# Performance work log

Measured on AMD Instinct MI355X. Metric: run time of the kernel, lower is better.

Reference implementation:

```python
import jax, jax.numpy as jnp
import numpy as np

N, D, K = 8192, 4096, 8
F_HID = D // 4  # 1024


def setup_inputs() -> dict:
    key = jax.random.key(0)
    ks = jax.random.split(key, 8)
    s1 = 1.0 / np.sqrt(2 * D)
    s2 = 1.0 / np.sqrt(F_HID)
    sr = 1.0 / np.sqrt(D)
    return {
        "h_anchor": jax.random.normal(ks[0], (N, D), jnp.float32),
        "h_mask": jax.random.normal(ks[1], (N, D), jnp.float32),
        "Wr": jax.random.normal(ks[2], (K, D), jnp.float32) * sr,
        "br": jnp.zeros((K,), jnp.float32),
        "W1": jax.random.normal(ks[3], (K, F_HID, 2 * D), jnp.float32) * s1,
        "b1": jnp.zeros((K, F_HID), jnp.float32),
        "W2": jax.random.normal(ks[4], (K, D, F_HID), jnp.float32) * s2,
        "b2": jnp.zeros((K, D), jnp.float32),
    }


def reference(h_anchor, h_mask, Wr, br, W1, b1, W2, b2):
    # routing weights: softmax(h_mask @ Wr^T + br) -> [N, K]
    weights = jax.nn.softmax(h_mask @ Wr.T + br, axis=-1)
    # conditioned input: [N, 2D]
    conditioned = jnp.concatenate([h_anchor, h_mask], axis=-1)
    # all-expert first GEMM: [K, N, F]
    h1 = jnp.einsum("nc,kfc->knf", conditioned, W1) + b1[:, None, :]
    h1 = jax.nn.gelu(h1, approximate=False)  # torch nn.GELU default = exact erf
    # second GEMM: [K, N, D]
    expert_out = jnp.einsum("knf,kdf->knd", h1, W2) + b2[:, None, :]
    # softmax-weighted combine over experts -> [N, D]
    return jnp.einsum("knd,nk->nd", expert_out, weights)
```

## Files before the change

### kernel.cpp

```cpp
#include <hip/hip_runtime.h>
#include <hip/hip_bf16.h>
#include <math.h>

typedef __bf16 bf16_t;
typedef __bf16 bf16x4 __attribute__((ext_vector_type(4)));
typedef __bf16 bf16x8 __attribute__((ext_vector_type(8)));
typedef float  f32x4  __attribute__((ext_vector_type(4)));
typedef float  f32x16 __attribute__((ext_vector_type(16)));

#define AS1 __attribute__((address_space(1)))
#define AS3 __attribute__((address_space(3)))

__device__ __forceinline__ void gload_lds16(const bf16_t* g, char* l) {
  __builtin_amdgcn_global_load_lds((const AS1 void*)g, (AS3 void*)l, 16, 0, 0);
}

static constexpr int N_ROWS = 8192;
static constexpr int DDIM   = 4096;
static constexpr int KEXP   = 8;
static constexpr int FHID   = 1024;
static constexpr int KD     = 8192;
static constexpr int NKT    = KD / 64;


__global__ __launch_bounds__(256)
void routing_kernel(const float* __restrict__ hm, const float* __restrict__ Wr,
                    const float* __restrict__ br, float* __restrict__ wgt) {
  const int n = blockIdx.x;
  const int t = threadIdx.x;
  const int wid = t >> 6;
  const float4* row = (const float4*)(hm + (size_t)n * DDIM);
  float4 x[4];
#pragma unroll
  for (int j = 0; j < 4; ++j) x[j] = row[t + j * 256];
  __shared__ float red[KEXP][4];
  float part[KEXP];
#pragma unroll
  for (int k = 0; k < KEXP; ++k) {
    const float4* wr = (const float4*)(Wr + (size_t)k * DDIM);
    float s = 0.f;
#pragma unroll
    for (int j = 0; j < 4; ++j) {
      float4 w4 = wr[t + j * 256];
      s += x[j].x * w4.x + x[j].y * w4.y + x[j].z * w4.z + x[j].w * w4.w;
    }
#pragma unroll
    for (int off = 32; off > 0; off >>= 1) s += __shfl_down(s, off);
    part[k] = s;
  }
  if ((t & 63) == 0) {
#pragma unroll
    for (int k = 0; k < KEXP; ++k) red[k][wid] = part[k];
  }
  __syncthreads();
  if (t == 0) {
    float lg[KEXP];
    float mx = -1e30f;
#pragma unroll
    for (int k = 0; k < KEXP; ++k) {
      lg[k] = red[k][0] + red[k][1] + red[k][2] + red[k][3] + br[k];
      mx = fmaxf(mx, lg[k]);
    }
    float sum = 0.f;
#pragma unroll
    for (int k = 0; k < KEXP; ++k) { lg[k] = expf(lg[k] - mx); sum += lg[k]; }
    float inv = 1.f / sum;
#pragma unroll
    for (int k = 0; k < KEXP; ++k) wgt[(size_t)n * KEXP + k] = lg[k] * inv;
  }
}

__device__ __forceinline__ bf16x4 cvt4(float4 v) {
  bf16x4 o;
  o[0] = (bf16_t)v.x; o[1] = (bf16_t)v.y; o[2] = (bf16_t)v.z; o[3] = (bf16_t)v.w;
  return o;
}

__global__ __launch_bounds__(256)
void pack_cond_kernel(const float* __restrict__ ha, const float* __restrict__ hm,
                      bf16_t* __restrict__ Apk) {
  const int bm = blockIdx.x >> 7, t = blockIdx.x & 127;
  const int tid = threadIdx.x;
  const float* src = (t < 64) ? ha : hm;
  const int cb = (t & 63) * 64;
  __shared__ char pb[32768];
#pragma unroll
  for (int i = 0; i < 16; ++i) {
    int u = i * 256 + tid;
    int r = u >> 4, c = (u & 15) * 4;
    float4 v = *(const float4*)(src + (size_t)(bm * 256 + r) * DDIM + cb + c);
    int off = ((r >> 7) & 1) * 16384 + ((c >> 4) & 3) * 4096 + ((r >> 5) & 3) * 1024
            + ((c >> 3) & 1) * 512 + (r & 31) * 16 + (c & 7) * 2;
    *(bf16x4*)(pb + off) = cvt4(v);
  }
  __syncthreads();
  char* dst = (char*)Apk + (size_t)blockIdx.x * 32768;
#pragma unroll
  for (int i = 0; i < 8; ++i) {
    int off = i * 4096 + tid * 16;
    *(float4*)(dst + off) = *(const float4*)(pb + off);
  }
}

__global__ __launch_bounds__(256)
void pack_w1_kernel(const float* __restrict__ W1, bf16_t* __restrict__ Bpk) {
  const int bn = blockIdx.x >> 7, t = blockIdx.x & 127;
  const int tid = threadIdx.x;
  __shared__ char pb[32768];
#pragma unroll
  for (int i = 0; i < 16; ++i) {
    int u = i * 256 + tid;
    int r = u >> 4, c = (u & 15) * 4;
    float4 v = *(const float4*)(W1 + (size_t)(bn * 256 + r) * KD + t * 64 + c);
    int off = ((c >> 4) & 3) * 8192 + ((r >> 5) & 7) * 1024
            + ((c >> 3) & 1) * 512 + (r & 31) * 16 + (c & 7) * 2;
    *(bf16x4*)(pb + off) = cvt4(v);
  }
  __syncthreads();
  char* dst = (char*)Bpk + (size_t)blockIdx.x * 32768;
#pragma unroll
  for (int i = 0; i < 8; ++i) {
    int off = i * 4096 + tid * 16;
    *(float4*)(dst + off) = *(const float4*)(pb + off);
  }
}

__global__ __launch_bounds__(256)
void pack_w2_kernel(const float* __restrict__ W2, bf16_t* __restrict__ Bpk) {
  const int bn = blockIdx.x >> 7, t = blockIdx.x & 127;
  const int tid = threadIdx.x;
  const int ke = t >> 4, f0 = (t & 15) * 64;
  __shared__ char pb[32768];
#pragma unroll
  for (int i = 0; i < 16; ++i) {
    int u = i * 256 + tid;
    int r = u >> 4, c = (u & 15) * 4;
    float4 v = *(const float4*)(W2 + ((size_t)ke * DDIM + bn * 256 + r) * FHID + f0 + c);
    int off = ((c >> 4) & 3) * 8192 + ((r >> 5) & 7) * 1024
            + ((c >> 3) & 1) * 512 + (r & 31) * 16 + (c & 7) * 2;
    *(bf16x4*)(pb + off) = cvt4(v);
  }
  __syncthreads();
  char* dst = (char*)Bpk + (size_t)blockIdx.x * 32768;
#pragma unroll
  for (int i = 0; i < 8; ++i) {
    int off = i * 4096 + tid * 16;
    *(float4*)(dst + off) = *(const float4*)(pb + off);
  }
}

template <int MODE, int NCOLS>
__global__ __launch_bounds__(512, 2)
void gemm256_kernel(const bf16_t* __restrict__ Apk, const bf16_t* __restrict__ Bpk,
                    void* __restrict__ Cout, const float* __restrict__ bias,
                    const float* __restrict__ wgt) {
  __shared__ char lds_raw[2 * 65536];

  const int tid  = threadIdx.x;
  const int wid  = tid >> 6;
  const int lane = tid & 63;
  const int wr   = wid >> 2;
  const int wc   = wid & 3;

  constexpr int NBN    = NCOLS / 256;
  constexpr int NWIN_N = NBN / 16;
  const int bid = blockIdx.x;
  const int w   = bid >> 8;
  const int sl  = bid & 255;
  const int xcd = sl & 7;
  const int cu  = sl >> 3;
  const int wm  = w / NWIN_N, wn = w % NWIN_N;
  const int bm  = wm * 16 + ((xcd >> 1) << 2) + (cu & 3);
  const int bn  = wn * 16 + ((xcd & 1) << 3) + (cu >> 2);
  const int arow0 = bm * 256;
  const int brow0 = bn * 256;

  const size_t abase = (size_t)bm * NKT * 16384;
  const size_t bbase = (size_t)bn * NKT * 16384;
  const size_t selo  = (size_t)(wid * 512 + lane * 8);
  const int    dsto  = wid << 10;

  f32x16 acc[4][2];
#pragma unroll
  for (int mi = 0; mi < 4; ++mi)
#pragma unroll
    for (int nj = 0; nj < 2; ++nj)
#pragma unroll
      for (int r = 0; r < 16; ++r) acc[mi][nj][r] = 0.f;

#define STG_A(I, TAU, NB)                                                        \
  gload_lds16(Apk + abase + (size_t)((TAU) & (NKT - 1)) * 16384 + (I) * 4096 + selo, \
              (NB) + (I) * 8192 + dsto);
#define STG_B(I, TAU, NB)                                                        \
  gload_lds16(Bpk + bbase + (size_t)((TAU) & (NKT - 1)) * 16384 + (I) * 4096 + selo, \
              (NB) + 32768 + (I) * 8192 + dsto);

  STG_A(0, 0, lds_raw) STG_A(2, 0, lds_raw) STG_B(0, 0, lds_raw) STG_B(1, 0, lds_raw)
  STG_A(1, 0, lds_raw) STG_A(3, 0, lds_raw) STG_B(2, 0, lds_raw) STG_B(3, 0, lds_raw)
  asm volatile("s_waitcnt vmcnt(0)" ::: "memory");
  __builtin_amdgcn_s_barrier();
  __builtin_amdgcn_sched_barrier(0);

#define SB __builtin_amdgcn_sched_barrier(0);
#define MM(MI)                                                                  \
    acc[MI][0] = __builtin_amdgcn_mfma_f32_32x32x16_bf16(aq[MI], qb0,           \
                                                         acc[MI][0], 0, 0, 0);  \
    acc[MI][1] = __builtin_amdgcn_mfma_f32_32x32x16_bf16(aq[MI], qb1,           \
                                                         acc[MI][1], 0, 0, 0);

#define PH(SS, STG0, STG1, GATE)                                                \
  {                                                                             \
    STG0;                                                                       \
    STG1;                                                                       \
    SB                                                                          \
    bf16x8 qb0 = *(const bf16x8*)(bB + (SS) * 8192);                            \
    bf16x8 qb1 = *(const bf16x8*)(bB + (SS) * 8192 + 1024);                     \
    SB                                                                          \
    bf16x8 aq[4];                                                               \
    aq[0] = *(const bf16x8*)(bA + (SS) * 4096);                                 \
    SB                                                                          \
    aq[1] = *(const bf16x8*)(bA + (SS) * 4096 + 1024);                          \
    SB                                                                          \
    aq[2] = *(const bf16x8*)(bA + (SS) * 4096 + 2048);                          \
    SB                                                                          \
    aq[3] = *(const bf16x8*)(bA + (SS) * 4096 + 3072);                          \
    SB                                                                          \
    __builtin_amdgcn_s_setprio(1);                                              \
    asm volatile("s_waitcnt lgkmcnt(3)" ::: "memory");                          \
    SB                                                                          \
    MM(0)                                                                       \
    SB                                                                          \
    asm volatile("s_waitcnt lgkmcnt(2)" ::: "memory");                          \
    SB                                                                          \
    MM(1)                                                                       \
    SB                                                                          \
    asm volatile("s_waitcnt lgkmcnt(1)" ::: "memory");                          \
    SB                                                                          \
    MM(2)                                                                       \
    SB                                                                          \
    asm volatile("s_waitcnt lgkmcnt(0)" ::: "memory");                          \
    SB                                                                          \
    MM(3)                                                                       \
    SB                                                                          \
    __builtin_amdgcn_s_setprio(0);                                              \
    if (GATE) {                                                                 \
      asm volatile("s_waitcnt vmcnt(4)" ::: "memory");                          \
      SB                                                                        \
      __builtin_amdgcn_s_barrier();                                             \
      SB                                                                        \
    }                                                                           \
  }

  int cur = 0;
  for (int t = 0; t < NKT; ++t) {
    char* nb = lds_raw + (cur ^ 65536);
    const char* bA = lds_raw + cur + wr * 16384 + lane * 16;
    const char* bB = lds_raw + cur + 32768 + wc * 2048 + lane * 16;
    PH(0, STG_A(0, t + 1, nb), STG_A(2, t + 1, nb), 0)
    PH(1, STG_B(0, t + 1, nb), STG_B(1, t + 1, nb), 1)
    PH(2, STG_A(1, t + 1, nb), STG_A(3, t + 1, nb), 0)
    PH(3, STG_B(2, t + 1, nb), STG_B(3, t + 1, nb), 1)
    cur ^= 65536;
  }
#undef PH
#undef MM
#undef SB
#undef STG_A
#undef STG_B

  const int rbase = arow0 + wr * 128 + ((lane >> 5) << 2);
  const int cbase = brow0 + wc * 64 + (lane & 31);

  if constexpr (MODE == 1) {
    char* __restrict__ Hc = (char*)Cout;
    const int kexp = brow0 >> 10;
    float bv[2] = {bias[cbase], bias[cbase + 32]};
    size_t cpart[2];
#pragma unroll
    for (int nj = 0; nj < 2; ++nj) {
      int c = cbase + nj * 32;
      cpart[nj] = (size_t)(c >> 6) * 32768 + ((c >> 4) & 3) * 4096
                + ((c >> 3) & 1) * 512 + (c & 7) * 2;
    }
#pragma unroll
    for (int mi = 0; mi < 4; ++mi)
#pragma unroll
      for (int r = 0; r < 16; ++r) {
        int n = rbase + mi * 32 + (r & 3) + 8 * (r >> 2);
        float wn4 = wgt[(size_t)n * KEXP + kexp];
        size_t npart = (size_t)(n >> 8) * (NKT * 32768) + ((n >> 7) & 1) * 16384
                     + ((n >> 5) & 3) * 1024 + (n & 31) * 16;
#pragma unroll
        for (int nj = 0; nj < 2; ++nj) {
          float x = acc[mi][nj][r] + bv[nj];
          float g = 0.5f * x * (1.f + erff(x * 0.70710678118654752f));
          *(bf16_t*)(Hc + npart + cpart[nj]) = (bf16_t)(g * wn4);
        }
      }
  } else {
    float* __restrict__ O = (float*)Cout;
    float bc0[KEXP], bc1[KEXP];
#pragma unroll
    for (int k = 0; k < KEXP; ++k) {
      bc0[k] = bias[(size_t)k * NCOLS + cbase];
      bc1[k] = bias[(size_t)k * NCOLS + cbase + 32];
    }
#pragma unroll
    for (int mi = 0; mi < 4; ++mi)
#pragma unroll
      for (int r = 0; r < 16; ++r) {
        int n = rbase + mi * 32 + (r & 3) + 8 * (r >> 2);
        const float4* wp = (const float4*)(wgt + (size_t)n * KEXP);
        float4 wa = wp[0], wb = wp[1];
        float w8[KEXP] = {wa.x, wa.y, wa.z, wa.w, wb.x, wb.y, wb.z, wb.w};
        float s0 = 0.f, s1 = 0.f;
#pragma unroll
        for (int k = 0; k < KEXP; ++k) { s0 += w8[k] * bc0[k]; s1 += w8[k] * bc1[k]; }
        O[(size_t)n * NCOLS + cbase]      = acc[mi][0][r] + s0;
        O[(size_t)n * NCOLS + cbase + 32] = acc[mi][1][r] + s1;
      }
  }
}

extern "C" void kernel_launch(void* const* d_in, const int* in_sizes, int n_in,
                              void* d_out, int out_size, void* d_ws, size_t ws_size,
                              hipStream_t stream) {
  const float* h_anchor = (const float*)d_in[0];
  const float* h_mask   = (const float*)d_in[1];
  const float* Wr       = (const float*)d_in[2];
  const float* br       = (const float*)d_in[3];
  const float* W1       = (const float*)d_in[4];
  const float* b1       = (const float*)d_in[5];
  const float* W2       = (const float*)d_in[6];
  const float* b2       = (const float*)d_in[7];
  float* out = (float*)d_out;

  char* ws = (char*)d_ws;
  bf16_t* Apk  = (bf16_t*)(ws);
  bf16_t* B1pk = (bf16_t*)(ws + ((size_t)128 << 20));
  bf16_t* B2pk = (bf16_t*)(ws + ((size_t)256 << 20));
  bf16_t* Hpk  = (bf16_t*)(ws + ((size_t)320 << 20));
  float*  wgt  = (float*) (ws + ((size_t)448 << 20));

  routing_kernel<<<N_ROWS, 256, 0, stream>>>(h_mask, Wr, br, wgt);
  pack_cond_kernel<<<32 * 128, 256, 0, stream>>>(h_anchor, h_mask, Apk);
  pack_w1_kernel<<<32 * 128, 256, 0, stream>>>(W1, B1pk);
  pack_w2_kernel<<<16 * 128, 256, 0, stream>>>(W2, B2pk);

  gemm256_kernel<1, 8192><<<(N_ROWS / 256) * (KD / 256), 512, 0, stream>>>(
      Apk, B1pk, (void*)Hpk, b1, wgt);
  gemm256_kernel<2, 4096><<<(N_ROWS / 256) * (DDIM / 256), 512, 0, stream>>>(
      Hpk, B2pk, (void*)out, b2, wgt);
}
```

Measured before the change: 1.639 ms.

## Use 4-wave blocks with 128x128 warp tiles and register double-buffered LDS reads

Halves the GEMM block to 256 threads (4 waves in a 2x2 grid), so each wave computes a 128x128 sub-tile with a 4x4 MFMA accumulator array instead of 4x2. LDS fragments are ping-ponged through two register sets (x/y), and the global-to-LDS staging for the next K tile is interleaved between MFMA groups, with one barrier per K tile. The aim is higher MFMA-to-LDS-read ratio and fewer barriers. In exchange it roughly doubles accumulator register pressure, leaves only 4 waves per CU for latency hiding, and drops the setprio hints.

```diff
diff --git a/kernel.cpp b/kernel.cpp
--- a/kernel.cpp
+++ b/kernel.cpp
@@ -150,7 +150,7 @@
 }
 
 template <int MODE, int NCOLS>
-__global__ __launch_bounds__(512, 2)
+__global__ __launch_bounds__(256, 1)
 void gemm256_kernel(const bf16_t* __restrict__ Apk, const bf16_t* __restrict__ Bpk,
                     void* __restrict__ Cout, const float* __restrict__ bias,
                     const float* __restrict__ wgt) {
@@ -159,8 +159,8 @@
   const int tid  = threadIdx.x;
   const int wid  = tid >> 6;
   const int lane = tid & 63;
-  const int wr   = wid >> 2;
-  const int wc   = wid & 3;
+  const int wr   = wid >> 1;
+  const int wc   = wid & 1;
 
   constexpr int NBN    = NCOLS / 256;
   constexpr int NWIN_N = NBN / 16;
@@ -177,108 +177,119 @@
 
   const size_t abase = (size_t)bm * NKT * 16384;
   const size_t bbase = (size_t)bn * NKT * 16384;
-  const size_t selo  = (size_t)(wid * 512 + lane * 8);
+  const size_t ssub  = (size_t)(wid * 512 + lane * 8);
   const int    dsto  = wid << 10;
 
-  f32x16 acc[4][2];
+  const char* A0 = lds_raw + wr * 16384 + lane * 16;
+  const char* B0 = lds_raw + 32768 + wc * 4096 + lane * 16;
+  const char* A1 = A0 + 65536;
+  const char* B1 = B0 + 65536;
+
+  f32x16 acc[4][4];
 #pragma unroll
   for (int mi = 0; mi < 4; ++mi)
 #pragma unroll
-    for (int nj = 0; nj < 2; ++nj)
+    for (int nj = 0; nj < 4; ++nj)
 #pragma unroll
       for (int r = 0; r < 16; ++r) acc[mi][nj][r] = 0.f;
 
-#define STG_A(I, TAU, NB)                                                        \
-  gload_lds16(Apk + abase + (size_t)((TAU) & (NKT - 1)) * 16384 + (I) * 4096 + selo, \
-              (NB) + (I) * 8192 + dsto);
-#define STG_B(I, TAU, NB)                                                        \
-  gload_lds16(Bpk + bbase + (size_t)((TAU) & (NKT - 1)) * 16384 + (I) * 4096 + selo, \
-              (NB) + 32768 + (I) * 8192 + dsto);
-
-  STG_A(0, 0, lds_raw) STG_A(2, 0, lds_raw) STG_B(0, 0, lds_raw) STG_B(1, 0, lds_raw)
-  STG_A(1, 0, lds_raw) STG_A(3, 0, lds_raw) STG_B(2, 0, lds_raw) STG_B(3, 0, lds_raw)
+  bf16x8 xa0, xa1, xa2, xa3, xb0, xb1, xb2, xb3;
+  bf16x8 ya0, ya1, ya2, ya3, yb0, yb1, yb2, yb3;
+
+#define SB __builtin_amdgcn_sched_barrier(0);
+#define LG0 asm volatile("s_waitcnt lgkmcnt(0)" ::: "memory"); SB
+
+#define STGA(C, TAU, NB)                                                         \
+  gload_lds16(Apk + abase + (size_t)((TAU) & (NKT - 1)) * 16384 + (C) * 2048 + ssub, \
+              (NB) + (C) * 4096 + dsto);
+#define STGB(C, TAU, NB)                                                         \
+  gload_lds16(Bpk + bbase + (size_t)((TAU) & (NKT - 1)) * 16384 + (C) * 2048 + ssub, \
+              (NB) + 32768 + (C) * 4096 + dsto);
+
+#define RDA4(P, BASE, S)                                                        \
+  P##a0 = *(const bf16x8*)((BASE) + (S) * 4096);                                \
+  P##a1 = *(const bf16x8*)((BASE) + (S) * 4096 + 1024);                         \
+  P##a2 = *(const bf16x8*)((BASE) + (S) * 4096 + 2048);                         \
+  P##a3 = *(const bf16x8*)((BASE) + (S) * 4096 + 3072);                         \
+  SB
+#define RDB4(P, BASE, S)                                                        \
+  P##b0 = *(const bf16x8*)((BASE) + (S) * 8192);                                \
+  P##b1 = *(const bf16x8*)((BASE) + (S) * 8192 + 1024);                         \
+  P##b2 = *(const bf16x8*)((BASE) + (S) * 8192 + 2048);                         \
+  P##b3 = *(const bf16x8*)((BASE) + (S) * 8192 + 3072);                         \
+  SB
+
+#define MF4(P, MI)                                                              \
+  acc[MI][0] = __builtin_amdgcn_mfma_f32_32x32x16_bf16(P##a##MI, P##b0,         \
+                                                       acc[MI][0], 0, 0, 0);    \
+  acc[MI][1] = __builtin_amdgcn_mfma_f32_32x32x16_bf16(P##a##MI, P##b1,         \
+                                                       acc[MI][1], 0, 0, 0);    \
+  acc[MI][2] = __builtin_amdgcn_mfma_f32_32x32x16_bf16(P##a##MI, P##b2,         \
+                                                       acc[MI][2], 0, 0, 0);    \
+  acc[MI][3] = __builtin_amdgcn_mfma_f32_32x32x16_bf16(P##a##MI, P##b3,         \
+                                                       acc[MI][3], 0, 0, 0);    \
+  SB
+
+#define TILE(T, CA, CB, NB)                                                     \
+  RDA4(x, CA, 0) RDB4(x, CB, 0)                                                 \
+  LG0                                                                           \
+  MF4(x, 0) RDA4(y, CA, 1)                                                      \
+  MF4(x, 1) RDB4(y, CB, 1)                                                      \
+  MF4(x, 2) STGA(0, (T) + 1, NB) STGA(1, (T) + 1, NB)                           \
+            STGA(2, (T) + 1, NB) STGA(3, (T) + 1, NB) SB                        \
+  MF4(x, 3) STGA(4, (T) + 1, NB) STGA(5, (T) + 1, NB)                           \
+            STGA(6, (T) + 1, NB) STGA(7, (T) + 1, NB) SB                        \
+  LG0                                                                           \
+  MF4(y, 0) RDA4(x, CA, 2)                                                      \
+  MF4(y, 1) RDB4(x, CB, 2)                                                      \
+  MF4(y, 2) STGB(0, (T) + 1, NB) STGB(1, (T) + 1, NB)                           \
+            STGB(2, (T) + 1, NB) STGB(3, (T) + 1, NB) SB                        \
+  MF4(y, 3) STGB(4, (T) + 1, NB) STGB(5, (T) + 1, NB)                           \
+            STGB(6, (T) + 1, NB) STGB(7, (T) + 1, NB) SB                        \
+  LG0                                                                           \
+  MF4(x, 0) RDA4(y, CA, 3)                                                      \
+  MF4(x, 1) RDB4(y, CB, 3)                                                      \
+  MF4(x, 2) MF4(x, 3)                                                           \
+  LG0                                                                           \
+  MF4(y, 0) MF4(y, 1) MF4(y, 2) MF4(y, 3)                                       \
+  asm volatile("s_waitcnt vmcnt(0)" ::: "memory");                              \
+  SB                                                                            \
+  __builtin_amdgcn_s_barrier();                                                 \
+  SB
+
+#pragma unroll
+  for (int c = 0; c < 8; ++c) { STGA(c, 0, lds_raw) }
+#pragma unroll
+  for (int c = 0; c < 8; ++c) { STGB(c, 0, lds_raw) }
   asm volatile("s_waitcnt vmcnt(0)" ::: "memory");
   __builtin_amdgcn_s_barrier();
-  __builtin_amdgcn_sched_barrier(0);
-
-#define SB __builtin_amdgcn_sched_barrier(0);
-#define MM(MI)                                                                  \
-    acc[MI][0] = __builtin_amdgcn_mfma_f32_32x32x16_bf16(aq[MI], qb0,           \
-                                                         acc[MI][0], 0, 0, 0);  \
-    acc[MI][1] = __builtin_amdgcn_mfma_f32_32x32x16_bf16(aq[MI], qb1,           \
-                                                         acc[MI][1], 0, 0, 0);
-
-#define PH(SS, STG0, STG1, GATE)                                                \
-  {                                                                             \
-    STG0;                                                                       \
-    STG1;                                                                       \
-    SB                                                                          \
-    bf16x8 qb0 = *(const bf16x8*)(bB + (SS) * 8192);                            \
-    bf16x8 qb1 = *(const bf16x8*)(bB + (SS) * 8192 + 1024);                     \
-    SB                                                                          \
-    bf16x8 aq[4];                                                               \
-    aq[0] = *(const bf16x8*)(bA + (SS) * 4096);                                 \
-    SB                                                                          \
-    aq[1] = *(const bf16x8*)(bA + (SS) * 4096 + 1024);                          \
-    SB                                                                          \
-    aq[2] = *(const bf16x8*)(bA + (SS) * 4096 + 2048);                          \
-    SB                                                                          \
-    aq[3] = *(const bf16x8*)(bA + (SS) * 4096 + 3072);                          \
-    SB                                                                          \
-    __builtin_amdgcn_s_setprio(1);                                              \
-    asm volatile("s_waitcnt lgkmcnt(3)" ::: "memory");                          \
-    SB                                                                          \
-    MM(0)                                                                       \
-    SB                                                                          \
-    asm volatile("s_waitcnt lgkmcnt(2)" ::: "memory");                          \
-    SB                                                                          \
-    MM(1)                                                                       \
-    SB                                                                          \
-    asm volatile("s_waitcnt lgkmcnt(1)" ::: "memory");                          \
-    SB                                                                          \
-    MM(2)                                                                       \
-    SB                                                                          \
-    asm volatile("s_waitcnt lgkmcnt(0)" ::: "memory");                          \
-    SB                                                                          \
-    MM(3)                                                                       \
-    SB                                                                          \
-    __builtin_amdgcn_s_setprio(0);                                              \
-    if (GATE) {                                                                 \
-      asm volatile("s_waitcnt vmcnt(4)" ::: "memory");                          \
-      SB                                                                        \
-      __builtin_amdgcn_s_barrier();                                             \
-      SB                                                                        \
-    }                                                                           \
-  }
-
-  int cur = 0;
-  for (int t = 0; t < NKT; ++t) {
-    char* nb = lds_raw + (cur ^ 65536);
-    const char* bA = lds_raw + cur + wr * 16384 + lane * 16;
-    const char* bB = lds_raw + cur + 32768 + wc * 2048 + lane * 16;
-    PH(0, STG_A(0, t + 1, nb), STG_A(2, t + 1, nb), 0)
-    PH(1, STG_B(0, t + 1, nb), STG_B(1, t + 1, nb), 1)
-    PH(2, STG_A(1, t + 1, nb), STG_A(3, t + 1, nb), 0)
-    PH(3, STG_B(2, t + 1, nb), STG_B(3, t + 1, nb), 1)
-    cur ^= 65536;
-  }
-#undef PH
-#undef MM
+  SB
+
+  for (int t = 0; t < NKT; t += 2) {
+    TILE(t, A0, B0, lds_raw + 65536)
+    TILE(t + 1, A1, B1, lds_raw)
+  }
+#undef TILE
+#undef MF4
+#undef RDA4
+#undef RDB4
+#undef STGA
+#undef STGB
+#undef LG0
 #undef SB
-#undef STG_A
-#undef STG_B
 
   const int rbase = arow0 + wr * 128 + ((lane >> 5) << 2);
-  const int cbase = brow0 + wc * 64 + (lane & 31);
+  const int cbase = brow0 + wc * 128 + (lane & 31);
 
   if constexpr (MODE == 1) {
     char* __restrict__ Hc = (char*)Cout;
     const int kexp = brow0 >> 10;
-    float bv[2] = {bias[cbase], bias[cbase + 32]};
-    size_t cpart[2];
-#pragma unroll
-    for (int nj = 0; nj < 2; ++nj) {
+    float bv[4];
+    size_t cpart[4];
+#pragma unroll
+    for (int nj = 0; nj < 4; ++nj) {
       int c = cbase + nj * 32;
+      bv[nj] = bias[c];
       cpart[nj] = (size_t)(c >> 6) * 32768 + ((c >> 4) & 3) * 4096
                 + ((c >> 3) & 1) * 512 + (c & 7) * 2;
     }
@@ -291,7 +302,7 @@
         size_t npart = (size_t)(n >> 8) * (NKT * 32768) + ((n >> 7) & 1) * 16384
                      + ((n >> 5) & 3) * 1024 + (n & 31) * 16;
 #pragma unroll
-        for (int nj = 0; nj < 2; ++nj) {
+        for (int nj = 0; nj < 4; ++nj) {
           float x = acc[mi][nj][r] + bv[nj];
           float g = 0.5f * x * (1.f + erff(x * 0.70710678118654752f));
           *(bf16_t*)(Hc + npart + cpart[nj]) = (bf16_t)(g * wn4);
@@ -299,12 +310,12 @@
       }
   } else {
     float* __restrict__ O = (float*)Cout;
-    float bc0[KEXP], bc1[KEXP];
-#pragma unroll
-    for (int k = 0; k < KEXP; ++k) {
-      bc0[k] = bias[(size_t)k * NCOLS + cbase];
-      bc1[k] = bias[(size_t)k * NCOLS + cbase + 32];
-    }
+    float bc[4][KEXP];
+#pragma unroll
+    for (int nj = 0; nj < 4; ++nj)
+#pragma unroll
+      for (int k = 0; k < KEXP; ++k)
+        bc[nj][k] = bias[(size_t)k * NCOLS + cbase + nj * 32];
 #pragma unroll
     for (int mi = 0; mi < 4; ++mi)
 #pragma unroll
@@ -313,11 +324,13 @@
         const float4* wp = (const float4*)(wgt + (size_t)n * KEXP);
         float4 wa = wp[0], wb = wp[1];
         float w8[KEXP] = {wa.x, wa.y, wa.z, wa.w, wb.x, wb.y, wb.z, wb.w};
-        float s0 = 0.f, s1 = 0.f;
-#pragma unroll
-        for (int k = 0; k < KEXP; ++k) { s0 += w8[k] * bc0[k]; s1 += w8[k] * bc1[k]; }
-        O[(size_t)n * NCOLS + cbase]      = acc[mi][0][r] + s0;
-        O[(size_t)n * NCOLS + cbase + 32] = acc[mi][1][r] + s1;
+#pragma unroll
+        for (int nj = 0; nj < 4; ++nj) {
+          float s = 0.f;
+#pragma unroll
+          for (int k = 0; k < KEXP; ++k) s += w8[k] * bc[nj][k];
+          O[(size_t)n * NCOLS + cbase + nj * 32] = acc[mi][nj][r] + s;
+        }
       }
   }
 }
@@ -347,8 +360,8 @@
   pack_w1_kernel<<<32 * 128, 256, 0, stream>>>(W1, B1pk);
   pack_w2_kernel<<<16 * 128, 256, 0, stream>>>(W2, B2pk);
 
-  gemm256_kernel<1, 8192><<<(N_ROWS / 256) * (KD / 256), 512, 0, stream>>>(
+  gemm256_kernel<1, 8192><<<(N_ROWS / 256) * (KD / 256), 256, 0, stream>>>(
       Apk, B1pk, (void*)Hpk, b1, wgt);
-  gemm256_kernel<2, 4096><<<(N_ROWS / 256) * (DDIM / 256), 512, 0, stream>>>(
+  gemm256_kernel<2, 4096><<<(N_ROWS / 256) * (DDIM / 256), 256, 0, stream>>>(
       Hpk, B2pk, (void*)out, b2, wgt);
 }
```

After: 1.789 ms. 1.09x slower.

## Load B operand directly from global into registers, stage only A in LDS

Applied to the files above, without the earlier changes.

The GEMM main loop stops staging the B tile in LDS. Each wave now reads its B fragments from global memory straight into registers, one k-tile ahead, while A keeps its double-buffered global-to-LDS path. This halves the LDS footprint, which could let a second workgroup fit per CU, and it cuts the loop to one barrier per k-tile. In exchange, waves that share a column group fetch the same B data redundantly from global/L2, global-load latency is exposed directly to the register operands, and the extra live B registers add pressure under the existing launch bounds.

```diff
diff --git a/kernel.cpp b/kernel.cpp
--- a/kernel.cpp
+++ b/kernel.cpp
@@ -154,7 +154,7 @@
 void gemm256_kernel(const bf16_t* __restrict__ Apk, const bf16_t* __restrict__ Bpk,
                     void* __restrict__ Cout, const float* __restrict__ bias,
                     const float* __restrict__ wgt) {
-  __shared__ char lds_raw[2 * 65536];
+  __shared__ char lds_raw[2 * 32768];
 
   const int tid  = threadIdx.x;
   const int wid  = tid >> 6;
@@ -175,10 +175,13 @@
   const int arow0 = bm * 256;
   const int brow0 = bn * 256;
 
-  const size_t abase = (size_t)bm * NKT * 16384;
-  const size_t bbase = (size_t)bn * NKT * 16384;
-  const size_t selo  = (size_t)(wid * 512 + lane * 8);
-  const int    dsto  = wid << 10;
+  const char* Ab = (const char*)Apk + (size_t)bm * NKT * 32768;
+  const char* Bb = (const char*)Bpk + (size_t)bn * NKT * 32768;
+
+  const int c0 = wid * 4;
+  const int bcg = wc * 2048 + lane * 16;
+  const char* bA0 = lds_raw + wr * 16384 + lane * 16;
+  const char* bA1 = bA0 + 32768;
 
   f32x16 acc[4][2];
 #pragma unroll
@@ -188,85 +191,73 @@
 #pragma unroll
       for (int r = 0; r < 16; ++r) acc[mi][nj][r] = 0.f;
 
-#define STG_A(I, TAU, NB)                                                        \
-  gload_lds16(Apk + abase + (size_t)((TAU) & (NKT - 1)) * 16384 + (I) * 4096 + selo, \
-              (NB) + (I) * 8192 + dsto);
-#define STG_B(I, TAU, NB)                                                        \
-  gload_lds16(Bpk + bbase + (size_t)((TAU) & (NKT - 1)) * 16384 + (I) * 4096 + selo, \
-              (NB) + 32768 + (I) * 8192 + dsto);
-
-  STG_A(0, 0, lds_raw) STG_A(2, 0, lds_raw) STG_B(0, 0, lds_raw) STG_B(1, 0, lds_raw)
-  STG_A(1, 0, lds_raw) STG_A(3, 0, lds_raw) STG_B(2, 0, lds_raw) STG_B(3, 0, lds_raw)
-  asm volatile("s_waitcnt vmcnt(0)" ::: "memory");
+  bf16x8 b0x, b0y, b1x, b1y, b2x, b2y, b3x, b3y;
+
+#define SB __builtin_amdgcn_sched_barrier(0);
+#define STG(I, TAU, NB)                                                          \
+  gload_lds16((const bf16_t*)(Ab + (size_t)((TAU) & (NKT - 1)) * 32768 +         \
+                              (c0 + (I)) * 1024 + lane * 16),                    \
+              (NB) + (c0 + (I)) * 1024);
+#define LDB(VAR, TAU, S, NJ)                                                     \
+  VAR = *(const bf16x8*)(Bb + (size_t)((TAU) & (NKT - 1)) * 32768 +              \
+                         (S) * 8192 + bcg + (NJ) * 1024);
+
+#define KSTEP(PA, BX, BY)                                                        \
+  {                                                                              \
+    bf16x8 aq0, aq1, aq2, aq3;                                                   \
+    aq0 = *(const bf16x8*)(PA);          SB                                      \
+    aq1 = *(const bf16x8*)((PA) + 1024); SB                                      \
+    aq2 = *(const bf16x8*)((PA) + 2048); SB                                      \
+    aq3 = *(const bf16x8*)((PA) + 3072); SB                                      \
+    __builtin_amdgcn_s_setprio(1);                                               \
+    acc[0][0] = __builtin_amdgcn_mfma_f32_32x32x16_bf16(aq0, BX, acc[0][0], 0, 0, 0); \
+    acc[0][1] = __builtin_amdgcn_mfma_f32_32x32x16_bf16(aq0, BY, acc[0][1], 0, 0, 0); \
+    SB                                                                           \
+    acc[1][0] = __builtin_amdgcn_mfma_f32_32x32x16_bf16(aq1, BX, acc[1][0], 0, 0, 0); \
+    acc[1][1] = __builtin_amdgcn_mfma_f32_32x32x16_bf16(aq1, BY, acc[1][1], 0, 0, 0); \
+    SB                                                                           \
+    acc[2][0] = __builtin_amdgcn_mfma_f32_32x32x16_bf16(aq2, BX, acc[2][0], 0, 0, 0); \
+    acc[2][1] = __builtin_amdgcn_mfma_f32_32x32x16_bf16(aq2, BY, acc[2][1], 0, 0, 0); \
+    SB                                                                           \
+    acc[3][0] = __builtin_amdgcn_mfma_f32_32x32x16_bf16(aq3, BX, acc[3][0], 0, 0, 0); \
+    acc[3][1] = __builtin_amdgcn_mfma_f32_32x32x16_bf16(aq3, BY, acc[3][1], 0, 0, 0); \
+    SB                                                                           \
+    __builtin_amdgcn_s_setprio(0);                                               \
+  }
+
+#define TILE(T, BA, NB)                                                          \
+  STG(0, (T) + 1, NB) STG(1, (T) + 1, NB) SB                                     \
+  LDB(b2x, (T), 2, 0) LDB(b2y, (T), 2, 1) SB                                     \
+  KSTEP((BA), b0x, b0y)                                                          \
+  STG(2, (T) + 1, NB) STG(3, (T) + 1, NB) SB                                     \
+  LDB(b3x, (T), 3, 0) LDB(b3y, (T), 3, 1) SB                                     \
+  KSTEP((BA) + 4096, b1x, b1y)                                                   \
+  LDB(b0x, (T) + 1, 0, 0) LDB(b0y, (T) + 1, 0, 1) SB                             \
+  KSTEP((BA) + 8192, b2x, b2y)                                                   \
+  LDB(b1x, (T) + 1, 1, 0) LDB(b1y, (T) + 1, 1, 1) SB                             \
+  KSTEP((BA) + 12288, b3x, b3y)                                                  \
+  asm volatile("s_waitcnt vmcnt(6)" ::: "memory");                               \
+  SB                                                                             \
+  __builtin_amdgcn_s_barrier();                                                  \
+  SB
+
+  STG(0, 0, lds_raw) STG(1, 0, lds_raw) STG(2, 0, lds_raw) STG(3, 0, lds_raw) SB
+  LDB(b0x, 0, 0, 0) LDB(b0y, 0, 0, 1) LDB(b1x, 0, 1, 0) LDB(b1y, 0, 1, 1) SB
+  asm volatile("s_waitcnt vmcnt(4)" ::: "memory");
+  SB
   __builtin_amdgcn_s_barrier();
-  __builtin_amdgcn_sched_barrier(0);
-
-#define SB __builtin_amdgcn_sched_barrier(0);
-#define MM(MI)                                                                  \
-    acc[MI][0] = __builtin_amdgcn_mfma_f32_32x32x16_bf16(aq[MI], qb0,           \
-                                                         acc[MI][0], 0, 0, 0);  \
-    acc[MI][1] = __builtin_amdgcn_mfma_f32_32x32x16_bf16(aq[MI], qb1,           \
-                                                         acc[MI][1], 0, 0, 0);
-
-#define PH(SS, STG0, STG1, GATE)                                                \
-  {                                                                             \
-    STG0;                                                                       \
-    STG1;                                                                       \
-    SB                                                                          \
-    bf16x8 qb0 = *(const bf16x8*)(bB + (SS) * 8192);                            \
-    bf16x8 qb1 = *(const bf16x8*)(bB + (SS) * 8192 + 1024);                     \
-    SB                                                                          \
-    bf16x8 aq[4];                                                               \
-    aq[0] = *(const bf16x8*)(bA + (SS) * 4096);                                 \
-    SB                                                                          \
-    aq[1] = *(const bf16x8*)(bA + (SS) * 4096 + 1024);                          \
-    SB                                                                          \
-    aq[2] = *(const bf16x8*)(bA + (SS) * 4096 + 2048);                          \
-    SB                                                                          \
-    aq[3] = *(const bf16x8*)(bA + (SS) * 4096 + 3072);                          \
-    SB                                                                          \
-    __builtin_amdgcn_s_setprio(1);                                              \
-    asm volatile("s_waitcnt lgkmcnt(3)" ::: "memory");                          \
-    SB                                                                          \
-    MM(0)                                                                       \
-    SB                                                                          \
-    asm volatile("s_waitcnt lgkmcnt(2)" ::: "memory");                          \
-    SB                                                                          \
-    MM(1)                                                                       \
-    SB                                                                          \
-    asm volatile("s_waitcnt lgkmcnt(1)" ::: "memory");                          \
-    SB                                                                          \
-    MM(2)                                                                       \
-    SB                                                                          \
-    asm volatile("s_waitcnt lgkmcnt(0)" ::: "memory");                          \
-    SB                                                                          \
-    MM(3)                                                                       \
-    SB                                                                          \
-    __builtin_amdgcn_s_setprio(0);                                              \
-    if (GATE) {                                                                 \
-      asm volatile("s_waitcnt vmcnt(4)" ::: "memory");                          \
-      SB                                                                        \
-      __builtin_amdgcn_s_barrier();                                             \
-      SB                                                                        \
-    }                                                                           \
-  }
-
-  int cur = 0;
-  for (int t = 0; t < NKT; ++t) {
-    char* nb = lds_raw + (cur ^ 65536);
-    const char* bA = lds_raw + cur + wr * 16384 + lane * 16;
-    const char* bB = lds_raw + cur + 32768 + wc * 2048 + lane * 16;
-    PH(0, STG_A(0, t + 1, nb), STG_A(2, t + 1, nb), 0)
-    PH(1, STG_B(0, t + 1, nb), STG_B(1, t + 1, nb), 1)
-    PH(2, STG_A(1, t + 1, nb), STG_A(3, t + 1, nb), 0)
-    PH(3, STG_B(2, t + 1, nb), STG_B(3, t + 1, nb), 1)
-    cur ^= 65536;
-  }
-#undef PH
-#undef MM
+  SB
+
+#pragma unroll 1
+  for (int t = 0; t < NKT; t += 2) {
+    TILE(t, bA0, lds_raw + 32768)
+    TILE(t + 1, bA1, lds_raw)
+  }
+#undef TILE
+#undef KSTEP
+#undef LDB
+#undef STG
 #undef SB
-#undef STG_A
-#undef STG_B
 
   const int rbase = arow0 + wr * 128 + ((lane >> 5) << 2);
   const int cbase = brow0 + wc * 64 + (lane & 31);
```

Measured after the change: 1.868 ms. 14.0% more time.
